# Kernel optimization log

Hardware: AMD Instinct MI355X
Metric: run time of the kernel (lower is better)

Reference implementation:

```python
import jax, jax.numpy as jnp
import numpy as np

B, S, D = 2, 2048, 1024
R = 64
H = 16
DH = D // H
N = 32  # neurons per bank (fqk, fv, rqk, rv)


def setup_inputs() -> dict:
    key = jax.random.key(0)
    ks = jax.random.split(key, 13)
    inp = {
        'x': jax.random.normal(ks[0], (B, S, D), dtype=jnp.float32),
        'fqk_weights_Q': jax.random.uniform(ks[1], (B, S, N), dtype=jnp.float32),
        'fqk_weights_K': jax.random.uniform(ks[2], (B, S, N), dtype=jnp.float32),
        'fv_weights': jax.random.uniform(ks[3], (B, S, N), dtype=jnp.float32),
        'rqk_weights_Q': jax.random.uniform(ks[4], (B, S, N), dtype=jnp.float32),
        'rqk_weights_K': jax.random.uniform(ks[5], (B, S, N), dtype=jnp.float32),
        'rv_weights': jax.random.uniform(ks[6], (B, S, N), dtype=jnp.float32),
        # neuron banks (orthogonal init in original; random normal is fine for numerics)
        'f_qk': jax.random.normal(ks[7], (N, D, R), dtype=jnp.float32) / np.sqrt(D),
        'f_v': jax.random.normal(ks[8], (N, D, R), dtype=jnp.float32) / np.sqrt(D),
        'r_qk': jax.random.normal(ks[9], (N, R, D), dtype=jnp.float32) / np.sqrt(R),
        'r_v': jax.random.normal(ks[10], (N, R, D), dtype=jnp.float32) / np.sqrt(R),
        'W_O': jax.random.normal(ks[11], (D, D), dtype=jnp.float32) / np.sqrt(D),  # torch Linear weight [out,in]
    }
    return inp


def _mix_project(x, w, neurons):
    # h[b,s,r] = sum_n w[b,s,n] * (x[b,s,:] @ neurons[n])  -- reassociated, avoids [B,S,D,R]
    p = jnp.einsum('bsd,ndr->bsnr', x, neurons)  # [B,S,N,R]
    return jnp.einsum('bsn,bsnr->bsr', w, p)


def _mix_restore(h, w, neurons):
    # y[b,s,d] = sum_n w[b,s,n] * (h[b,s,:] @ neurons[n])  -- reassociated, avoids [B,S,R,D]
    hw = jnp.einsum('bsr,bsn->bsnr', h, w)  # [B,S,N,R]
    return jnp.einsum('bsnr,nrd->bsd', hw, neurons)


def _causal_sdpa(Q, K, V):
    # Q,K,V: [B,H,S,DH]
    scale = 1.0 / np.sqrt(Q.shape[-1]).astype(np.float32)
    scores = jnp.einsum('bhqd,bhkd->bhqk', Q, K) * scale
    s = Q.shape[2]
    mask = jnp.tril(jnp.ones((s, s), dtype=bool))
    scores = jnp.where(mask, scores, jnp.finfo(scores.dtype).min)
    attn = jax.nn.softmax(scores, axis=-1)
    return jnp.einsum('bhqk,bhkd->bhqd', attn, V)


def reference(x, fqk_weights_Q, fqk_weights_K, fv_weights,
              rqk_weights_Q, rqk_weights_K, rv_weights,
              f_qk, f_v, r_qk, r_v, W_O):
    b, s, d = x.shape
    h_q = _mix_project(x, fqk_weights_Q, f_qk)  # [B,S,R]
    h_k = _mix_project(x, fqk_weights_K, f_qk)
    h_v = _mix_project(x, fv_weights, f_v)

    Q = _mix_restore(h_q, rqk_weights_Q, r_qk)  # [B,S,D]
    K = _mix_restore(h_k, rqk_weights_K, r_qk)
    V = _mix_restore(h_v, rv_weights, r_v)

    Q = Q.reshape(b, s, H, DH).transpose(0, 2, 1, 3)
    K = K.reshape(b, s, H, DH).transpose(0, 2, 1, 3)
    V = V.reshape(b, s, H, DH).transpose(0, 2, 1, 3)

    attn_out = _causal_sdpa(Q, K, V)  # [B,H,S,DH]
    attn_out = attn_out.transpose(0, 2, 1, 3).reshape(b, s, d)
    out = attn_out @ W_O.T  # nn.Linear(d, d, bias=False)
    return out
```

## Files before the change

### kernel.cpp

```cpp
#include <hip/hip_runtime.h>
#include <hip/hip_bf16.h>
#include <cstdint>
#include <cstddef>

typedef unsigned short u16;
typedef short bfrag __attribute__((ext_vector_type(8)));
typedef _Float16 hfrag __attribute__((ext_vector_type(8)));
typedef float f32x4 __attribute__((ext_vector_type(4)));
typedef u16 u16x8 __attribute__((ext_vector_type(8)));

__device__ __forceinline__ u16 f2bf(float v) {
    union { float f; unsigned u; } a; a.f = v;
    unsigned r = a.u + 0x7fff + ((a.u >> 16) & 1);
    return (u16)(r >> 16);
}
__device__ __forceinline__ float bf2f(u16 u) {
    union { unsigned u; float f; } a; a.u = ((unsigned)u) << 16;
    return a.f;
}
__device__ __forceinline__ u16 f2h(float v) {
    union { _Float16 h; u16 u; } a; a.h = (_Float16)v;
    return a.u;
}
__device__ __forceinline__ f32x4 mfma_bf16(bfrag a, bfrag b, f32x4 c) {
    return __builtin_amdgcn_mfma_f32_16x16x32_bf16(a, b, c, 0, 0, 0);
}
__device__ __forceinline__ f32x4 mfma_f16(hfrag a, hfrag b, f32x4 c) {
    return __builtin_amdgcn_mfma_f32_16x16x32_f16(a, b, c, 0, 0, 0);
}
__device__ __forceinline__ void async_copy16(const void* g, void* l) {
    __builtin_amdgcn_global_load_lds(
        (const __attribute__((address_space(1))) unsigned*)g,
        (__attribute__((address_space(3))) unsigned*)l, 16, 0, 0);
}
__device__ __forceinline__ int get_xcd() {
    unsigned x;
    asm volatile("s_getreg_b32 %0, hwreg(HW_REG_XCC_ID)" : "=s"(x));
    return (int)(x & 7);
}

template<int SPLIT>
__global__ __launch_bounds__(256) void cast_split(const float* __restrict__ s,
                                                  u16* __restrict__ dh,
                                                  u16* __restrict__ dl, int n4)
{
    int i = blockIdx.x * 256 + threadIdx.x;
    if (i >= n4) return;
    float4 v = ((const float4*)s)[i];
    float vv[4] = {v.x, v.y, v.z, v.w};
    ushort4 h, l;
    u16* hp = (u16*)&h; u16* lp = (u16*)&l;
#pragma unroll
    for (int e = 0; e < 4; ++e) {
        u16 hb = f2bf(vv[e]);
        hp[e] = hb;
        if (SPLIT) lp[e] = f2bf(vv[e] - bf2f(hb));
    }
    ((ushort4*)dh)[i] = h;
    if (SPLIT) ((ushort4*)dl)[i] = l;
}

template<int MODE>
__global__ __launch_bounds__(256) void transpose_cast(const float* __restrict__ src,
                                                      u16* __restrict__ dh,
                                                      u16* __restrict__ dl,
                                                      int R, int C, int dpitch)
{
    __shared__ float t[32][33];
    int z = blockIdx.z;
    const float* s = src + (size_t)z * R * C;
    int r0 = blockIdx.y * 32, c0 = blockIdx.x * 32;
    int tx = threadIdx.x & 31, ty = threadIdx.x >> 5;
#pragma unroll
    for (int p = 0; p < 4; ++p)
        t[ty + p * 8][tx] = s[(size_t)(r0 + ty + p * 8) * C + c0 + tx];
    __syncthreads();
#pragma unroll
    for (int p = 0; p < 4; ++p) {
        int rr = ty + p * 8;
        float v = t[tx][rr];
        size_t di = (size_t)(z * C + c0 + rr) * dpitch + r0 + tx;
        if (MODE == 2) {
            dh[di] = f2h(v);
        } else {
            u16 hb = f2bf(v);
            dh[di] = hb;
            if (MODE == 1) dl[di] = f2bf(v - bf2f(hb));
        }
    }
}

template<int SPLIT, int CTH>
__global__ __launch_bounds__(256) void gemm_mfma(const u16* __restrict__ Agh,
                                                 const u16* __restrict__ Agl,
                                                 const u16* __restrict__ Bgh,
                                                 const u16* __restrict__ Bgl,
                                                 float* __restrict__ C,
                                                 int M, int N, int K)
{
    constexpr int HB = SPLIT ? 16384 : 8192;
    __shared__ u16 lds[2 * HB];

    const int bid = blockIdx.x;
    const int idx = bid >> 3;
    const int ct  = (bid & 7) + 8 * (idx % CTH);
    const int rowt = idx / CTH;
    const int row0 = rowt * 128;
    const int col0 = ct * 128;

    const int tid  = threadIdx.x;
    const int lane = tid & 63;
    const int wv   = tid >> 6;
    const int q    = lane >> 4;
    const int tn   = lane & 15;
    const int wm   = (wv >> 1) * 64;
    const int wn   = (wv & 1) * 64;
    const int wbase = (tid & 192) * 8;

    auto stage = [&](u16* base, int k0) {
        u16* Ath = base;
        u16* Atl = SPLIT ? (base + 4096) : base;
        u16* Bth = base + (SPLIT ? 8192 : 4096);
        u16* Btl = SPLIT ? (base + 12288) : base;
#pragma unroll
        for (int shot = 0; shot < 2; ++shot) {
            int G = tid + shot * 256;
            int row = G >> 2, kgs = G & 3;
            int kgg = kgs ^ ((row >> 1) & 3);
            size_t goffB = (size_t)(col0 + row) * K + k0 + kgg * 8;
            async_copy16(Bgh + goffB, Bth + shot * 2048 + wbase);
            if (SPLIT) async_copy16(Bgl + goffB, Btl + shot * 2048 + wbase);
            size_t goffA = (size_t)(row0 + row) * K + k0 + kgg * 8;
            async_copy16(Agh + goffA, Ath + shot * 2048 + wbase);
            if (SPLIT) async_copy16(Agl + goffA, Atl + shot * 2048 + wbase);
        }
    };

    f32x4 acc[4][4];
#pragma unroll
    for (int i = 0; i < 4; ++i)
#pragma unroll
        for (int j = 0; j < 4; ++j) acc[i][j] = 0.f;

    stage(lds, 0);
    __syncthreads();

    int cur = 0;
    const int NT = K >> 5;
    for (int n = 0; n < NT; ++n) {
        if (n + 1 < NT) stage(lds + (cur ^ 1) * HB, (n + 1) * 32);

        const u16* base = lds + cur * HB;
        const u16* Ath = base;
        const u16* Atl = SPLIT ? (base + 4096) : base;
        const u16* Bth = base + (SPLIT ? 8192 : 4096);
        const u16* Btl = SPLIT ? (base + 12288) : base;

        bfrag ah[4], bh[4], al[4], bl[4];
#pragma unroll
        for (int i = 0; i < 4; ++i) {
            int m = wm + i * 16 + tn;
            int g = m * 4 + (q ^ ((m >> 1) & 3));
            ah[i] = *(const bfrag*)(Ath + g * 8);
            if (SPLIT) al[i] = *(const bfrag*)(Atl + g * 8);
        }
#pragma unroll
        for (int j = 0; j < 4; ++j) {
            int n2 = wn + j * 16 + tn;
            int g = n2 * 4 + (q ^ ((n2 >> 1) & 3));
            bh[j] = *(const bfrag*)(Bth + g * 8);
            if (SPLIT) bl[j] = *(const bfrag*)(Btl + g * 8);
        }
#pragma unroll
        for (int i = 0; i < 4; ++i)
#pragma unroll
            for (int j = 0; j < 4; ++j) {
                acc[i][j] = mfma_bf16(ah[i], bh[j], acc[i][j]);
                if (SPLIT) {
                    acc[i][j] = mfma_bf16(ah[i], bl[j], acc[i][j]);
                    acc[i][j] = mfma_bf16(al[i], bh[j], acc[i][j]);
                }
            }
        __syncthreads();
        cur ^= 1;
    }

#pragma unroll
    for (int i = 0; i < 4; ++i)
#pragma unroll
        for (int j = 0; j < 4; ++j)
#pragma unroll
            for (int rg = 0; rg < 4; ++rg) {
                int row = row0 + wm + i * 16 + q * 4 + rg;
                int col = col0 + wn + j * 16 + tn;
                C[(size_t)row * N + col] = acc[i][j][rg];
            }
}

__global__ __launch_bounds__(256) void build_ahw(
    const float* __restrict__ h_q, const float* __restrict__ wQ,
    const float* __restrict__ h_k, const float* __restrict__ wK,
    const float* __restrict__ h_v, const float* __restrict__ wV,
    u16* __restrict__ Ahw)
{
    const int b   = blockIdx.x;
    const int sel = b >> 12;
    const int row = b & 4095;
    const float* h = (sel == 0) ? h_q : (sel == 1) ? h_k : h_v;
    const float* w = (sel == 0) ? wQ  : (sel == 1) ? wK  : wV;
    const int kg = threadIdx.x;
    const float wm = w[(size_t)row * 32 + (kg >> 3)];
    const float* hp = h + (size_t)row * 64 + (kg & 7) * 8;
    float4 v0 = *(const float4*)hp;
    float4 v1 = *(const float4*)(hp + 4);
    float vv[8] = {v0.x, v0.y, v0.z, v0.w, v1.x, v1.y, v1.z, v1.w};
    u16x8 o;
#pragma unroll
    for (int e = 0; e < 8; ++e) o[e] = f2h(vv[e] * wm);
    *(u16x8*)(Ahw + (((size_t)sel * 4096 + row) * 2048) + kg * 8) = o;
}

__global__ __launch_bounds__(256) void restore_mega(
    const u16* __restrict__ Ahw,
    const u16* __restrict__ Rqk, const u16* __restrict__ Rv,
    u16* __restrict__ Qf, u16* __restrict__ Kf, u16* __restrict__ Vt,
    int* __restrict__ queue)
{
    __shared__ int sjob;
    __shared__ u16 lds[2][8192];

    const int tid = threadIdx.x;
    if (tid == 0) {
        int xcd = get_xcd();
        int job = -1;
        for (int t = 0; t < 8; ++t) {
            int qi = (xcd + t) & 7;
            int j = atomicAdd(&queue[qi], 1);
            if (j < 96) { job = qi * 96 + j; break; }
        }
        sjob = job;
    }
    __syncthreads();
    const int job = sjob;
    if (job < 0) return;
    const int ct   = job / 96;
    const int jj   = job % 96;
    const int sel  = jj >> 5;
    const int rowt = jj & 31;
    const u16* Ag = Ahw + (size_t)sel * 4096 * 2048;
    const u16* Bg = (sel < 2) ? Rqk : Rv;
    const int K = 2048;
    const int row0 = rowt * 128, col0 = ct * 128;

    const int lane = tid & 63;
    const int wv   = tid >> 6;
    const int q    = lane >> 4;
    const int tn   = lane & 15;
    const int wm   = (wv >> 1) * 64;
    const int wn   = (wv & 1) * 64;
    const int wbase = (tid & 192) * 8;

    auto stage = [&](u16* base, int k0) {
        u16* Ath = base;
        u16* Bth = base + 4096;
#pragma unroll
        for (int shot = 0; shot < 2; ++shot) {
            int G = tid + shot * 256;
            int row = G >> 2, kgs = G & 3;
            int kgg = kgs ^ ((row >> 1) & 3);
            size_t goffB = (size_t)(col0 + row) * K + k0 + kgg * 8;
            async_copy16(Bg + goffB, Bth + shot * 2048 + wbase);
            size_t goffA = (size_t)(row0 + row) * K + k0 + kgg * 8;
            async_copy16(Ag + goffA, Ath + shot * 2048 + wbase);
        }
    };

    f32x4 acc[4][4];
#pragma unroll
    for (int i = 0; i < 4; ++i)
#pragma unroll
        for (int j = 0; j < 4; ++j) acc[i][j] = 0.f;

    stage(lds[0], 0);
    __syncthreads();

    int cur = 0;
    for (int n = 0; n < 64; ++n) {
        if (n + 1 < 64) stage(lds[cur ^ 1], (n + 1) * 32);

        const u16* Ath = lds[cur];
        const u16* Bth = lds[cur] + 4096;

        hfrag ah[4], bh[4];
#pragma unroll
        for (int i = 0; i < 4; ++i) {
            int m = wm + i * 16 + tn;
            int g = m * 4 + (q ^ ((m >> 1) & 3));
            ah[i] = *(const hfrag*)(Ath + g * 8);
        }
#pragma unroll
        for (int j = 0; j < 4; ++j) {
            int n2 = wn + j * 16 + tn;
            int g = n2 * 4 + (q ^ ((n2 >> 1) & 3));
            bh[j] = *(const hfrag*)(Bth + g * 8);
        }
#pragma unroll
        for (int i = 0; i < 4; ++i)
#pragma unroll
            for (int j = 0; j < 4; ++j)
                acc[i][j] = mfma_f16(ah[i], bh[j], acc[i][j]);
        __syncthreads();
        cur ^= 1;
    }

#pragma unroll
    for (int i = 0; i < 4; ++i)
#pragma unroll
        for (int j = 0; j < 4; ++j)
#pragma unroll
            for (int rg = 0; rg < 4; ++rg) {
                int row = row0 + wm + i * 16 + q * 4 + rg;
                int col = col0 + wn + j * 16 + tn;
                float v = acc[i][j][rg];
                if (sel < 2) {
                    size_t ix = (((size_t)(row >> 11) * 16 + (col >> 6)) << 17)
                              | ((size_t)(row & 2047) << 6) | (size_t)(col & 63);
                    ((sel == 0) ? Qf : Kf)[ix] = f2h(v);
                } else {
                    size_t ix = ((((size_t)(row >> 11) * 16 + (col >> 6)) * 64
                                 + (size_t)(col & 63)) << 11) | (size_t)(row & 2047);
                    Vt[ix] = f2h(v);
                }
            }
}

__global__ __launch_bounds__(256) void mix_kernel(const float* __restrict__ P,
                                                  const float* __restrict__ w1,
                                                  const float* __restrict__ w2,
                                                  float* __restrict__ h1,
                                                  float* __restrict__ h2,
                                                  int two)
{
    int tid = blockIdx.x * 256 + threadIdx.x;
    int bs = tid >> 6;
    int r  = tid & 63;
    const float* Pp = P + (size_t)bs * 2048 + r;
    float a = 0.f, b = 0.f;
#pragma unroll
    for (int n = 0; n < 32; ++n) {
        float p = Pp[n * 64];
        a = fmaf(w1[bs * 32 + n], p, a);
        if (two) b = fmaf(w2[bs * 32 + n], p, b);
    }
    h1[tid] = a;
    if (two) h2[tid] = b;
}

template<int SHOTS>
__device__ __forceinline__ void stage_tile(u16* dst, const u16* src, int rowstride,
                                           int tid, int wuni)
{
#pragma unroll
    for (int shot = 0; shot < SHOTS; ++shot) {
        int sl = shot * 256 + tid;
        int m = sl >> 3, s = sl & 7, g = s ^ (m & 7);
        async_copy16(src + (size_t)m * rowstride + g * 8, dst + shot * 2048 + wuni);
    }
}

__global__ __launch_bounds__(256) void flash_part(const u16* __restrict__ Qf_g,
                                                  const u16* __restrict__ Kf_g,
                                                  const u16* __restrict__ Vt_g,
                                                  u16* __restrict__ Opart,
                                                  float* __restrict__ ml)
{
    const int bid = blockIdx.x;
    const int idx = bid >> 3;
    const int bh  = (bid & 7) + 8 * (idx & 3);
    const int rest = idx >> 2;
    const int qb = 31 - (rest >> 3);
    const int c  = rest & 7;
    const int g  = qb >> 2, rr = qb & 3;
    const int nch = g + 1;
    if (c >= nch) return;
    const int q0 = qb * 64;
    const int slot = bh * 144 + (qb + 2 * g * (g - 1) + rr * g) + c;

    const int tid = threadIdx.x;
    const int lane = tid & 63;
    const int wv = tid >> 6;
    const int q = lane >> 4;
    const int tn = lane & 15;
    const int wuni = (tid & 192) * 8;

    __shared__ u16 sQ[4096], sK[4096], sV[4096], sP[4096];

    const size_t qoff = ((size_t)bh * 2048 + q0) * 64;
    stage_tile<2>(sQ, Qf_g + qoff, 64, tid, wuni);
    __syncthreads();

    hfrag qf[2];
#pragma unroll
    for (int ks = 0; ks < 2; ++ks) {
        int m = wv * 16 + tn;
        int slt = (ks * 4 + q) ^ (m & 7);
        qf[ks] = *(const hfrag*)(sQ + m * 64 + slt * 8);
    }

    float m_i[4], l_i[4];
    f32x4 acc_o[4];
#pragma unroll
    for (int ri = 0; ri < 4; ++ri) { m_i[ri] = -3.0e38f; l_i[ri] = 0.f; }
#pragma unroll
    for (int dt = 0; dt < 4; ++dt) acc_o[dt] = 0.f;

    const size_t kbase = (size_t)bh * 2048 * 64;
    const size_t vbase = (size_t)bh * 64 * 2048;
    const int kt_end = min(4 * c + 3, qb);

    for (int kt = 4 * c; kt <= kt_end; ++kt) {
        const int k0 = kt * 64;
        __syncthreads();
        stage_tile<2>(sK, Kf_g + kbase + (size_t)k0 * 64, 64, tid, wuni);
        stage_tile<2>(sV, Vt_g + vbase + k0, 2048, tid, wuni);
        __syncthreads();

        f32x4 accs[4];
#pragma unroll
        for (int n = 0; n < 4; ++n) accs[n] = 0.f;
#pragma unroll
        for (int n = 0; n < 4; ++n) {
            int r = n * 16 + tn;
#pragma unroll
            for (int ks = 0; ks < 2; ++ks) {
                int slt = (ks * 4 + q) ^ (r & 7);
                hfrag kf = *(const hfrag*)(sK + r * 64 + slt * 8);
                accs[n] = mfma_f16(qf[ks], kf, accs[n]);
            }
        }
        const bool diag = (kt == qb);
#pragma unroll
        for (int n = 0; n < 4; ++n)
#pragma unroll
            for (int ri = 0; ri < 4; ++ri) {
                float v = accs[n][ri] * 0.125f;
                if (diag && (n * 16 + tn > wv * 16 + q * 4 + ri)) v = -3.0e38f;
                accs[n][ri] = v;
            }
        float alpha[4], mnew[4], ssum[4];
#pragma unroll
        for (int ri = 0; ri < 4; ++ri) {
            float mx = fmaxf(fmaxf(accs[0][ri], accs[1][ri]),
                             fmaxf(accs[2][ri], accs[3][ri]));
#pragma unroll
            for (int xm = 1; xm < 16; xm <<= 1)
                mx = fmaxf(mx, __shfl_xor(mx, xm, 64));
            mnew[ri] = fmaxf(m_i[ri], mx);
            alpha[ri] = __expf(m_i[ri] - mnew[ri]);
            m_i[ri] = mnew[ri];
            ssum[ri] = 0.f;
        }
#pragma unroll
        for (int n = 0; n < 4; ++n)
#pragma unroll
            for (int ri = 0; ri < 4; ++ri) {
                float p = __expf(accs[n][ri] - mnew[ri]);
                ssum[ri] += p;
                int m = wv * 16 + q * 4 + ri;
                int cc = n * 16 + tn;
                int slt = (cc >> 3) ^ (m & 7);
                sP[m * 64 + slt * 8 + (cc & 7)] = f2h(p);
            }
#pragma unroll
        for (int ri = 0; ri < 4; ++ri) {
            float sm = ssum[ri];
#pragma unroll
            for (int xm = 1; xm < 16; xm <<= 1)
                sm += __shfl_xor(sm, xm, 64);
            l_i[ri] = l_i[ri] * alpha[ri] + sm;
#pragma unroll
            for (int dt = 0; dt < 4; ++dt) acc_o[dt][ri] *= alpha[ri];
        }
#pragma unroll
        for (int ks = 0; ks < 2; ++ks) {
            int m = wv * 16 + tn;
            int slt = (ks * 4 + q) ^ (m & 7);
            hfrag pf = *(const hfrag*)(sP + m * 64 + slt * 8);
#pragma unroll
            for (int dt = 0; dt < 4; ++dt) {
                int d = dt * 16 + tn;
                int vslt = (ks * 4 + q) ^ (d & 7);
                hfrag vf = *(const hfrag*)(sV + d * 64 + vslt * 8);
                acc_o[dt] = mfma_f16(pf, vf, acc_o[dt]);
            }
        }
    }

#pragma unroll
    for (int dt = 0; dt < 4; ++dt)
#pragma unroll
        for (int ri = 0; ri < 4; ++ri) {
            int row = wv * 16 + q * 4 + ri;
            Opart[(size_t)slot * 4096 + row * 64 + dt * 16 + tn] = f2bf(acc_o[dt][ri]);
        }
    if (tn == 0) {
#pragma unroll
        for (int ri = 0; ri < 4; ++ri) {
            int row = wv * 16 + q * 4 + ri;
            ml[(size_t)slot * 128 + row]      = m_i[ri];
            ml[(size_t)slot * 128 + 64 + row] = l_i[ri];
        }
    }
}

__global__ __launch_bounds__(256) void flash_combine(const u16* __restrict__ Opart,
                                                     const float* __restrict__ ml,
                                                     u16* __restrict__ Am)
{
    const int qb = blockIdx.x, bh = blockIdx.y;
    const int g = qb >> 2, rr = qb & 3;
    const int nch = g + 1;
    const int base = bh * 144 + (qb + 2 * g * (g - 1) + rr * g);
    const int tid = threadIdx.x;
    const int row = tid >> 2;
    const int c0  = (tid & 3) * 16;

    float mstar = -3.0e38f;
    float mc[8];
#pragma unroll
    for (int c = 0; c < 8; ++c) {
        if (c < nch) {
            mc[c] = ml[(size_t)(base + c) * 128 + row];
            mstar = fmaxf(mstar, mc[c]);
        }
    }
    float lstar = 0.f, wc[8];
#pragma unroll
    for (int c = 0; c < 8; ++c) {
        if (c < nch) {
            wc[c] = __expf(mc[c] - mstar);
            lstar += ml[(size_t)(base + c) * 128 + 64 + row] * wc[c];
        }
    }
    float o[16];
#pragma unroll
    for (int j = 0; j < 16; ++j) o[j] = 0.f;
    for (int c = 0; c < nch; ++c) {
        const u16* p = Opart + (size_t)(base + c) * 4096 + row * 64 + c0;
        u16x8 v0 = *(const u16x8*)p;
        u16x8 v1 = *(const u16x8*)(p + 8);
#pragma unroll
        for (int j = 0; j < 8; ++j) {
            o[j]     = fmaf(bf2f(v0[j]), wc[c], o[j]);
            o[j + 8] = fmaf(bf2f(v1[j]), wc[c], o[j + 8]);
        }
    }
    float inv = 1.0f / lstar;
    int srow = qb * 64 + row;
    size_t obase = ((size_t)(bh >> 4) * 2048 + srow) * 1024
                 + (size_t)((bh & 15) * 64 + c0);
    u16x8 w0, w1;
#pragma unroll
    for (int j = 0; j < 8; ++j) {
        w0[j] = f2bf(o[j] * inv);
        w1[j] = f2bf(o[j + 8] * inv);
    }
    *(u16x8*)(Am + obase)     = w0;
    *(u16x8*)(Am + obase + 8) = w1;
}

extern "C" void kernel_launch(void* const* d_in, const int* in_sizes, int n_in,
                              void* d_out, int out_size, void* d_ws, size_t ws_size,
                              hipStream_t stream)
{
    const float* x     = (const float*)d_in[0];
    const float* wfqkQ = (const float*)d_in[1];
    const float* wfqkK = (const float*)d_in[2];
    const float* wfv   = (const float*)d_in[3];
    const float* wrqkQ = (const float*)d_in[4];
    const float* wrqkK = (const float*)d_in[5];
    const float* wrv   = (const float*)d_in[6];
    const float* f_qk  = (const float*)d_in[7];
    const float* f_v   = (const float*)d_in[8];
    const float* r_qk  = (const float*)d_in[9];
    const float* r_v   = (const float*)d_in[10];
    const float* W_O   = (const float*)d_in[11];
    float* out = (float*)d_out;

    const size_t MB = 1u << 20;
    char* w8 = (char*)d_ws;
    u16*  WOb   = (u16*)(w8 + 0);
    u16*  x_hi  = (u16*)(w8 + 2  * MB);
    u16*  x_lo  = (u16*)(w8 + 10 * MB);
    u16*  FqkTh = (u16*)(w8 + 18 * MB);
    u16*  FqkTl = (u16*)(w8 + 22 * MB);
    u16*  FvT   = (u16*)(w8 + 26 * MB);
    u16*  RqkT  = (u16*)(w8 + 30 * MB);
    u16*  RvT   = (u16*)(w8 + 34 * MB);
    float* h_q  = (float*)(w8 + 38 * MB);
    float* h_k  = (float*)(w8 + 39 * MB);
    float* h_v  = (float*)(w8 + 40 * MB);
    int*  queue = (int*)(w8 + 41 * MB);
    u16*  Ahw   = (u16*)(w8 + 42 * MB);
    float* P    = (float*)(w8 + 48 * MB);
    u16*  Qf    = (u16*)(w8 + 2  * MB);
    u16*  Kf    = (u16*)(w8 + 10 * MB);
    u16*  Vt    = (u16*)(w8 + 18 * MB);
    u16*  Opart = (u16*)(w8 + 28 * MB);
    float* mlws = (float*)(w8 + 64 * MB);
    u16*  Am    = (u16*)(w8 + 67 * MB);

    dim3 blk(256);

    cast_split<1><<<dim3(4096), blk, 0, stream>>>(x, x_hi, x_lo, 1024 * 1024);
    cast_split<0><<<dim3(1024), blk, 0, stream>>>(W_O, WOb, nullptr, 256 * 1024);
    transpose_cast<1><<<dim3(2, 32, 32), blk, 0, stream>>>(f_qk, FqkTh, FqkTl, 1024, 64, 1024);
    transpose_cast<0><<<dim3(2, 32, 32), blk, 0, stream>>>(f_v,  FvT,   nullptr, 1024, 64, 1024);
    transpose_cast<2><<<dim3(32, 64, 1), blk, 0, stream>>>(r_qk, RqkT, nullptr, 2048, 1024, 2048);
    transpose_cast<2><<<dim3(32, 64, 1), blk, 0, stream>>>(r_v,  RvT,  nullptr, 2048, 1024, 2048);

    gemm_mfma<1, 2><<<dim3(512), blk, 0, stream>>>(x_hi, x_lo, FqkTh, FqkTl, P,
                                                   4096, 2048, 1024);
    mix_kernel<<<dim3(1024), blk, 0, stream>>>(P, wfqkQ, wfqkK, h_q, h_k, 1);
    gemm_mfma<0, 2><<<dim3(512), blk, 0, stream>>>(x_hi, nullptr, FvT, nullptr, P,
                                                   4096, 2048, 1024);
    mix_kernel<<<dim3(1024), blk, 0, stream>>>(P, wfv, nullptr, h_v, nullptr, 0);

    build_ahw<<<dim3(3 * 4096), blk, 0, stream>>>(h_q, wrqkQ, h_k, wrqkK, h_v, wrv, Ahw);
    hipMemsetAsync(queue, 0, 8 * sizeof(int), stream);
    restore_mega<<<dim3(768), blk, 0, stream>>>(Ahw, RqkT, RvT, Qf, Kf, Vt, queue);

    flash_part<<<dim3(8192), blk, 0, stream>>>(Qf, Kf, Vt, Opart, mlws);
    flash_combine<<<dim3(32, 32), blk, 0, stream>>>(Opart, mlws, Am);

    gemm_mfma<0, 1><<<dim3(256), blk, 0, stream>>>(Am, nullptr, WOb, nullptr, out,
                                                   4096, 1024, 1024);
}
```

Measured before the change: 431.5 us.

## Remap GEMM and restore tiles per XCD for L2 reuse; single-buffer restore LDS

The generic GEMM's block-to-tile mapping now gives each XCD (bid&7) a contiguous band of row tiles, iterating column tiles within it. The aim is for one XCD's blocks to share A rows in their private L2. restore_mega's work-queue jobs are remapped the same way: each XCD queue owns a group of (sel,row) tiles and walks all 8 column tiles, so the A operand stays in that XCD's L2 instead of B columns. The restore kernel also drops LDS double buffering for a single buffer with sync-after-load. That halves LDS per block, which may raise occupancy, but it exposes load latency because loads no longer overlap the MFMAs.

```diff
diff --git a/kernel.cpp b/kernel.cpp
--- a/kernel.cpp
+++ b/kernel.cpp
@@ -102,9 +102,11 @@
     __shared__ u16 lds[2 * HB];
 
     const int bid = blockIdx.x;
-    const int idx = bid >> 3;
-    const int ct  = (bid & 7) + 8 * (idx % CTH);
-    const int rowt = idx / CTH;
+    const int xq  = bid & 7;
+    const int s   = bid >> 3;
+    const int RP  = (M >> 7) >> 3;
+    const int rowt = xq * RP + (s % RP);
+    const int ct   = s / RP;
     const int row0 = rowt * 128;
     const int col0 = ct * 128;
 
@@ -227,7 +229,9 @@
     int* __restrict__ queue)
 {
     __shared__ int sjob;
-    __shared__ u16 lds[2][8192];
+    __shared__ u16 lds[8192];
+    u16* Ath = lds;
+    u16* Bth = lds + 4096;
 
     const int tid = threadIdx.x;
     if (tid == 0) {
@@ -243,10 +247,12 @@
     __syncthreads();
     const int job = sjob;
     if (job < 0) return;
-    const int ct   = job / 96;
-    const int jj   = job % 96;
-    const int sel  = jj >> 5;
-    const int rowt = jj & 31;
+    const int qi   = job / 96;
+    const int j    = job % 96;
+    const int p    = qi * 12 + (j >> 3);
+    const int sel  = p >> 5;
+    const int rowt = p & 31;
+    const int ct   = j & 7;
     const u16* Ag = Ahw + (size_t)sel * 4096 * 2048;
     const u16* Bg = (sel < 2) ? Rqk : Rv;
     const int K = 2048;
@@ -260,9 +266,13 @@
     const int wn   = (wv & 1) * 64;
     const int wbase = (tid & 192) * 8;
 
-    auto stage = [&](u16* base, int k0) {
-        u16* Ath = base;
-        u16* Bth = base + 4096;
+    f32x4 acc[4][4];
+#pragma unroll
+    for (int i = 0; i < 4; ++i)
+#pragma unroll
+        for (int jj2 = 0; jj2 < 4; ++jj2) acc[i][jj2] = 0.f;
+
+    for (int k0 = 0; k0 < K; k0 += 32) {
 #pragma unroll
         for (int shot = 0; shot < 2; ++shot) {
             int G = tid + shot * 256;
@@ -273,23 +283,7 @@
             size_t goffA = (size_t)(row0 + row) * K + k0 + kgg * 8;
             async_copy16(Ag + goffA, Ath + shot * 2048 + wbase);
         }
-    };
-
-    f32x4 acc[4][4];
-#pragma unroll
-    for (int i = 0; i < 4; ++i)
-#pragma unroll
-        for (int j = 0; j < 4; ++j) acc[i][j] = 0.f;
-
-    stage(lds[0], 0);
-    __syncthreads();
-
-    int cur = 0;
-    for (int n = 0; n < 64; ++n) {
-        if (n + 1 < 64) stage(lds[cur ^ 1], (n + 1) * 32);
-
-        const u16* Ath = lds[cur];
-        const u16* Bth = lds[cur] + 4096;
+        __syncthreads();
 
         hfrag ah[4], bh[4];
 #pragma unroll
@@ -299,29 +293,28 @@
             ah[i] = *(const hfrag*)(Ath + g * 8);
         }
 #pragma unroll
-        for (int j = 0; j < 4; ++j) {
-            int n2 = wn + j * 16 + tn;
-            int g = n2 * 4 + (q ^ ((n2 >> 1) & 3));
-            bh[j] = *(const hfrag*)(Bth + g * 8);
+        for (int jj2 = 0; jj2 < 4; ++jj2) {
+            int n = wn + jj2 * 16 + tn;
+            int g = n * 4 + (q ^ ((n >> 1) & 3));
+            bh[jj2] = *(const hfrag*)(Bth + g * 8);
         }
 #pragma unroll
         for (int i = 0; i < 4; ++i)
 #pragma unroll
-            for (int j = 0; j < 4; ++j)
-                acc[i][j] = mfma_f16(ah[i], bh[j], acc[i][j]);
+            for (int jj2 = 0; jj2 < 4; ++jj2)
+                acc[i][jj2] = mfma_f16(ah[i], bh[jj2], acc[i][jj2]);
         __syncthreads();
-        cur ^= 1;
     }
 
 #pragma unroll
     for (int i = 0; i < 4; ++i)
 #pragma unroll
-        for (int j = 0; j < 4; ++j)
+        for (int jj2 = 0; jj2 < 4; ++jj2)
 #pragma unroll
             for (int rg = 0; rg < 4; ++rg) {
                 int row = row0 + wm + i * 16 + q * 4 + rg;
-                int col = col0 + wn + j * 16 + tn;
-                float v = acc[i][j][rg];
+                int col = col0 + wn + jj2 * 16 + tn;
+                float v = acc[i][jj2][rg];
                 if (sel < 2) {
                     size_t ix = (((size_t)(row >> 11) * 16 + (col >> 6)) << 17)
                               | ((size_t)(row & 2047) << 6) | (size_t)(col & 63);
```

Result: faster. 411.5 us (-4.6%).
